# Kernel tuning notes

Hardware: AMD Instinct MI355X
Metric: run time of the kernel (lower is better)

## Reference

```python
import jax, jax.numpy as jnp
import numpy as np

N = 2_000_000
VOXEL_SIZE = (0.1, 0.1, 0.1)
PC_RANGE = (-50.0, -50.0, -5.0, 50.0, 50.0, 3.0)
NUM_BATCHES = 4


def setup_inputs() -> dict:
    key = jax.random.key(0)
    k1, k2 = jax.random.split(key)
    pmin = jnp.array(PC_RANGE[:3], dtype=jnp.float32)
    pmax = jnp.array(PC_RANGE[3:], dtype=jnp.float32)
    # points uniformly distributed over the configured point-cloud range
    points = jax.random.uniform(k1, (N, 3), dtype=jnp.float32, minval=pmin, maxval=pmax)
    batch_indices = jnp.sort(jax.random.randint(k2, (N,), 0, NUM_BATCHES, dtype=jnp.int32))
    return {"points": points, "batch_indices": batch_indices}


def reference(points, batch_indices):
    """Vectorized equivalent of PointVoxelizer.forward.

    Returns fixed-shape (jit-friendly) analogues of the torch outputs:
      voxel_coords   [N, 4] int32  [batch, z, y, x], padded rows = -1
      voxel_features [N, 3] float32 voxel centers, padded rows = 0
      point_to_voxel_map [N] int32, -1 for invalid points
      n_voxels       scalar int32, number of real (non-padding) voxels
    The per-batch torch.unique + offset concatenation is reproduced exactly by
    a single sorted unique over the combined hash batch*GRID + cell_hash,
    since unique sorts and the hash is lexicographic in (batch, x, y, z).
    """
    dtype = points.dtype
    vsize = jnp.array(VOXEL_SIZE, dtype=dtype)
    pmin = jnp.array(PC_RANGE[:3], dtype=dtype)
    pmax = jnp.array(PC_RANGE[3:], dtype=dtype)

    vc = jnp.floor((points - pmin) / vsize).astype(jnp.int32)  # [N,3] (x,y,z)
    grid = jnp.ceil((pmax - pmin) / vsize).astype(jnp.int32)   # [3] = (1000,1000,80)
    valid = jnp.all(vc >= 0, axis=1) & jnp.all(vc < grid, axis=1)  # [N]

    YZ = grid[1] * grid[2]
    GXYZ = grid[0] * YZ  # cells per batch element (8e7 < 2^31/NUM_BATCHES)
    cell_hash = vc[:, 0] * YZ + vc[:, 1] * grid[2] + vc[:, 2]
    SENTINEL = jnp.iinfo(jnp.int32).max
    combined = jnp.where(valid, batch_indices.astype(jnp.int32) * GXYZ + cell_hash, SENTINEL)

    uniq, inv = jnp.unique(combined, return_inverse=True, size=N, fill_value=SENTINEL)
    is_real = uniq != SENTINEL  # padding (and any invalid-point bucket) masked out

    point_to_voxel_map = jnp.where(valid, inv.reshape(-1).astype(jnp.int32), -1)

    b = uniq // GXYZ
    rem = uniq % GXYZ
    x = rem // YZ
    y = (rem % YZ) // grid[2]
    z = rem % grid[2]

    coords_bzyx = jnp.stack([b, z, y, x], axis=1).astype(jnp.int32)  # [N,4]
    voxel_coords = jnp.where(is_real[:, None], coords_bzyx, -1)

    xyz = jnp.stack([x, y, z], axis=1).astype(dtype)
    centers = pmin + (xyz + 0.5) * vsize
    voxel_features = jnp.where(is_real[:, None], centers, jnp.zeros((), dtype))

    n_voxels = is_real.sum().astype(jnp.int32)
    return voxel_coords, voxel_features, point_to_voxel_map, n_voxels
```

## Files before the change

kernel.cpp:

```cpp
#include <hip/hip_runtime.h>


namespace {

constexpr int GX = 1000, GY = 1000, GZ = 80;
constexpr int YZ = GY * GZ;
constexpr int GXYZ = GX * YZ;
constexpr int TOTAL_CELLS = GXYZ * 4;
constexpr int BBITS = 18;
constexpr int BCELLS = 1 << BBITS;
constexpr int NB = (TOTAL_CELLS + BCELLS - 1) >> BBITS;
constexpr int BWORDS = BCELLS / 32;
constexpr int NCHUNK = 1024;
static_assert(NCHUNK % 64 == 0, "k2a wave scan");

constexpr size_t OFF_PK   = 8000000;
constexpr size_t OFF_POS  = 16000000;
constexpr size_t OFF_MVAL = 24000000;
constexpr size_t OFF_HIST = 32000000;
constexpr size_t OFF_TOT  = 38000000;
constexpr size_t OFF_BOFF = 38100000;
constexpr size_t OFF_DCNT = 38200000;

__device__ __forceinline__ int sw(int w) {
  return ((w & 7) << 10) | (w >> 3);
}

__global__ void k1_keys_hist(const float* __restrict__ pts, const int* __restrict__ bi,
                             unsigned* __restrict__ upt, unsigned* __restrict__ hist,
                             int n, int cpb) {
  __shared__ unsigned h[NB];
  const int c = blockIdx.x;
  for (int b = threadIdx.x; b < NB; b += blockDim.x) h[b] = 0;
  __syncthreads();
  const int lo = c * cpb, hi = min(n, lo + cpb);
  for (int i = lo + threadIdx.x; i < hi; i += blockDim.x) {
    float px = pts[3 * i + 0], py = pts[3 * i + 1], pz = pts[3 * i + 2];
    int vx = (int)floorf((px + 50.0f) / 0.1f);
    int vy = (int)floorf((py + 50.0f) / 0.1f);
    int vz = (int)floorf((pz + 5.0f) / 0.1f);
    bool valid = (vx >= 0) & (vy >= 0) & (vz >= 0) & (vx < GX) & (vy < GY) & (vz < GZ);
    unsigned u = 0xFFFFFFFFu;
    if (valid) {
      u = (unsigned)(bi[i] * GXYZ + vx * YZ + vy * GZ + vz);
      atomicAdd(&h[u >> BBITS], 1u);
    }
    upt[i] = u;
  }
  __syncthreads();
  for (int b = threadIdx.x; b < NB; b += blockDim.x)
    hist[(size_t)c * NB + b] = h[b];
}

__global__ void k2a_chunk_pre(unsigned* __restrict__ hist, unsigned* __restrict__ tot) {
  const int wid = (blockIdx.x * blockDim.x + threadIdx.x) >> 6;
  const int lane = threadIdx.x & 63;
  if (wid >= NB) return;
  unsigned run = 0;
  for (int c0 = 0; c0 < NCHUNK; c0 += 64) {
    const size_t idx = (size_t)(c0 + lane) * NB + wid;
    unsigned v = hist[idx];
    unsigned inc = v;
    for (int o = 1; o < 64; o <<= 1) {
      unsigned t = __shfl_up(inc, o);
      if (lane >= o) inc += t;
    }
    hist[idx] = run + inc - v;
    run += __shfl(inc, 63);
  }
  if (lane == 63) tot[wid] = run;
}

__global__ void k2b_scan_tot(const unsigned* __restrict__ tot, unsigned* __restrict__ boff) {
  __shared__ unsigned s[1024];
  const int tid = threadIdx.x;
  unsigned v0 = (2 * tid     < NB) ? tot[2 * tid]     : 0u;
  unsigned v1 = (2 * tid + 1 < NB) ? tot[2 * tid + 1] : 0u;
  unsigned t = v0 + v1;
  s[tid] = t;
  __syncthreads();
  for (int o = 1; o < 1024; o <<= 1) {
    unsigned add = (tid >= o) ? s[tid - o] : 0u;
    __syncthreads();
    s[tid] += add;
    __syncthreads();
  }
  unsigned excl = s[tid] - t;
  if (2 * tid     < NB) boff[2 * tid]     = excl;
  if (2 * tid + 1 < NB) boff[2 * tid + 1] = excl + v0;
  if (tid == 1023) boff[NB] = s[1023];
}

__global__ void k3_scatter(const unsigned* __restrict__ upt, const unsigned* __restrict__ hist,
                           const unsigned* __restrict__ boff, unsigned* __restrict__ pk,
                           unsigned* __restrict__ pos, int n, int cpb) {
  __shared__ unsigned cur[NB];
  const int c = blockIdx.x;
  for (int b = threadIdx.x; b < NB; b += blockDim.x)
    cur[b] = boff[b] + hist[(size_t)c * NB + b];
  __syncthreads();
  const int lo = c * cpb, hi = min(n, lo + cpb);
  for (int i = lo + threadIdx.x; i < hi; i += blockDim.x) {
    unsigned u = upt[i];
    if (u == 0xFFFFFFFFu) continue;
    unsigned p = atomicAdd(&cur[u >> BBITS], 1u);
    pk[p] = u;
    pos[i] = p;
  }
}

__global__ void __launch_bounds__(1024) k4_count(const unsigned* __restrict__ pk,
                                                 const unsigned* __restrict__ boff,
                                                 unsigned* __restrict__ dcnt) {
  __shared__ unsigned bits[BWORDS];
  __shared__ unsigned red[1024];
  const int b = blockIdx.x, tid = threadIdx.x;
  for (int w = tid; w < BWORDS; w += 1024) bits[w] = 0;
  __syncthreads();
  const unsigned lo = boff[b], hi = boff[b + 1];
  const unsigned base = (unsigned)b << BBITS;
  for (unsigned p = lo + tid; p < hi; p += 1024) {
    unsigned local = pk[p] - base;
    atomicOr(&bits[local >> 5], 1u << (local & 31));
  }
  __syncthreads();
  unsigned cnt = 0;
  for (int w = tid; w < BWORDS; w += 1024) cnt += __popc(bits[w]);
  red[tid] = cnt;
  __syncthreads();
  for (int o = 512; o > 0; o >>= 1) {
    if (tid < o) red[tid] += red[tid + o];
    __syncthreads();
  }
  if (tid == 0) dcnt[b] = red[0];
}

__global__ void __launch_bounds__(1024) k6_emit(
    const unsigned* __restrict__ pk, const unsigned* __restrict__ boff,
    const unsigned* __restrict__ dcnt, float* __restrict__ out_coords,
    float* __restrict__ out_feats, float* __restrict__ mapval,
    float* __restrict__ out_nvox, int n) {
  __shared__ unsigned bits[BWORDS];
  __shared__ unsigned wpre[BWORDS];
  __shared__ unsigned s[1024];
  const int tid = threadIdx.x;
  const int bid = blockIdx.x;

  if (bid >= NB) {
    unsigned part = 0;
    for (int k = tid; k < NB; k += 1024) part += dcnt[k];
    s[tid] = part;
    __syncthreads();
    for (int o = 512; o > 0; o >>= 1) {
      if (tid < o) s[tid] += s[tid + o];
      __syncthreads();
    }
    const unsigned nv = s[0];
    if (bid == NB && tid == 0) *out_nvox = (float)nv;
    const int row = (bid - NB) * 1024 + tid;
    if (row < n && (unsigned)row >= nv) {
      float* c = out_coords + (size_t)row * 4;
      c[0] = -1.0f; c[1] = -1.0f; c[2] = -1.0f; c[3] = -1.0f;
      float* f = out_feats + (size_t)row * 3;
      f[0] = 0.0f; f[1] = 0.0f; f[2] = 0.0f;
    }
    return;
  }

  unsigned part = 0;
  for (int k = tid; k < bid; k += 1024) part += dcnt[k];
  s[tid] = part;
  __syncthreads();
  for (int o = 512; o > 0; o >>= 1) {
    if (tid < o) s[tid] += s[tid + o];
    __syncthreads();
  }
  const unsigned drank = s[0];
  __syncthreads();

  for (int w = tid; w < BWORDS; w += 1024) bits[w] = 0;
  __syncthreads();
  const unsigned lo = boff[bid], hi = boff[bid + 1];
  const unsigned base = (unsigned)bid << BBITS;
  for (unsigned p = lo + tid; p < hi; p += 1024) {
    unsigned local = pk[p] - base;
    atomicOr(&bits[sw(local >> 5)], 1u << (local & 31));
  }
  __syncthreads();

  unsigned c8[8];
  unsigned t = 0;
  #pragma unroll
  for (int j = 0; j < 8; j++) {
    unsigned p = __popc(bits[j * 1024 + tid]);
    c8[j] = t;
    t += p;
  }
  s[tid] = t;
  __syncthreads();
  for (int o = 1; o < 1024; o <<= 1) {
    unsigned add = (tid >= o) ? s[tid - o] : 0u;
    __syncthreads();
    s[tid] += add;
    __syncthreads();
  }
  const unsigned excl = s[tid] - t;
  #pragma unroll
  for (int j = 0; j < 8; j++) wpre[j * 1024 + tid] = excl + c8[j];
  __syncthreads();

  #pragma unroll
  for (int j = 0; j < 8; j++) {
    const int slot = j * 1024 + tid;
    unsigned m = bits[slot];
    unsigned r = drank + wpre[slot];
    const unsigned lbase = (unsigned)(tid * 8 + j) << 5;
    while (m) {
      int bit = __ffs(m) - 1;
      m &= m - 1;
      unsigned u = base + lbase + (unsigned)bit;
      int bat = (int)(u / (unsigned)GXYZ);
      int rem = (int)(u % (unsigned)GXYZ);
      int x = rem / YZ, ry = rem % YZ;
      int y = ry / GZ, z = ry % GZ;
      float* cc = out_coords + (size_t)r * 4;
      cc[0] = (float)bat; cc[1] = (float)z; cc[2] = (float)y; cc[3] = (float)x;
      float* ff = out_feats + (size_t)r * 3;
      ff[0] = -50.0f + ((float)x + 0.5f) * 0.1f;
      ff[1] = -50.0f + ((float)y + 0.5f) * 0.1f;
      ff[2] = -5.0f + ((float)z + 0.5f) * 0.1f;
      r++;
    }
  }

  for (unsigned p = lo + tid; p < hi; p += 1024) {
    unsigned local = pk[p] - base;
    int slot = sw((int)(local >> 5));
    unsigned r = drank + wpre[slot] + (unsigned)__popc(bits[slot] & ((1u << (local & 31)) - 1u));
    mapval[p] = (float)r;
  }
}

__global__ void k7_map(const unsigned* __restrict__ upt, const unsigned* __restrict__ pos,
                       const float* __restrict__ mapval, float* __restrict__ out_map, int n) {
  int i = blockIdx.x * blockDim.x + threadIdx.x;
  if (i >= n) return;
  unsigned u = upt[i];
  if (u == 0xFFFFFFFFu) {
    out_map[i] = -1.0f;
    return;
  }
  out_map[i] = mapval[pos[i]];
}

}

extern "C" void kernel_launch(void* const* d_in, const int* in_sizes, int n_in,
                              void* d_out, int out_size, void* d_ws, size_t ws_size,
                              hipStream_t stream) {
  const int N = in_sizes[0] / 3;
  const float* pts = (const float*)d_in[0];
  const int* bi = (const int*)d_in[1];
  float* out = (float*)d_out;

  unsigned* upt = (unsigned*)d_ws;
  unsigned* pk   = (unsigned*)((char*)d_ws + OFF_PK);
  unsigned* pos  = (unsigned*)((char*)d_ws + OFF_POS);
  float*    mval = (float*)((char*)d_ws + OFF_MVAL);
  unsigned* hist = (unsigned*)((char*)d_ws + OFF_HIST);
  unsigned* tot  = (unsigned*)((char*)d_ws + OFF_TOT);
  unsigned* boff = (unsigned*)((char*)d_ws + OFF_BOFF);
  unsigned* dcnt = (unsigned*)((char*)d_ws + OFF_DCNT);

  float* out_coords = out;
  float* out_feats  = out + 4LL * N;
  float* out_map    = out + 7LL * N;
  float* out_nvox   = out + 8LL * N;

  const int cpb = (N + NCHUNK - 1) / NCHUNK;
  const int pad_blocks = (N + 1023) / 1024;

  k1_keys_hist<<<NCHUNK, 256, 0, stream>>>(pts, bi, upt, hist, N, cpb);
  k2a_chunk_pre<<<(NB * 64 + 255) / 256, 256, 0, stream>>>(hist, tot);
  k2b_scan_tot<<<1, 1024, 0, stream>>>(tot, boff);
  k3_scatter<<<NCHUNK, 256, 0, stream>>>(upt, hist, boff, pk, pos, N, cpb);
  k4_count<<<NB, 1024, 0, stream>>>(pk, boff, dcnt);
  k6_emit<<<NB + pad_blocks, 1024, 0, stream>>>(pk, boff, dcnt, out_coords,
                                                out_feats, mval, out_nvox, N);
  k7_map<<<(N + 1023) / 1024, 1024, 0, stream>>>(upt, pos, mval, out_map, N);
}
```

Measured before the change: 197.9 us.

## Merge count and rank passes, compute local ranks, defer global offset to emit

Drops the separate count kernel, which rebuilt each bucket's occupancy bitmap just to count distinct cells. The rank kernel now builds the bitmap once, writes its distinct count plus bucket-local ranks and the sorted distinct keys to workspace. A new lighter emit kernel adds the global prefix and decodes coordinates. The map kernel adds a per-bucket rank from a table. NCHUNK is halved and block sizes shrink to 256. This costs an extra global write and read of the distinct keys and a table lookup per point.

```diff
diff --git a/kernel.cpp b/kernel.cpp
--- a/kernel.cpp
+++ b/kernel.cpp
@@ -11,16 +11,18 @@
 constexpr int BCELLS = 1 << BBITS;
 constexpr int NB = (TOTAL_CELLS + BCELLS - 1) >> BBITS;
 constexpr int BWORDS = BCELLS / 32;
-constexpr int NCHUNK = 1024;
+constexpr int NCHUNK = 512;
 static_assert(NCHUNK % 64 == 0, "k2a wave scan");
 
-constexpr size_t OFF_PK   = 8000000;
-constexpr size_t OFF_POS  = 16000000;
-constexpr size_t OFF_MVAL = 24000000;
-constexpr size_t OFF_HIST = 32000000;
-constexpr size_t OFF_TOT  = 38000000;
-constexpr size_t OFF_BOFF = 38100000;
-constexpr size_t OFF_DCNT = 38200000;
+constexpr size_t OFF_PK    = 8000000;
+constexpr size_t OFF_POS   = 16000000;
+constexpr size_t OFF_MVAL  = 24000000;
+constexpr size_t OFF_DK    = 32000000;
+constexpr size_t OFF_HIST  = 40000000;
+constexpr size_t OFF_TOT   = 43000000;
+constexpr size_t OFF_BOFF  = 43100000;
+constexpr size_t OFF_DCNT  = 43200000;
+constexpr size_t OFF_DRANK = 43300000;
 
 __device__ __forceinline__ int sw(int w) {
   return ((w & 7) << 10) | (w >> 3);
@@ -109,74 +111,15 @@
   }
 }
 
-__global__ void __launch_bounds__(1024) k4_count(const unsigned* __restrict__ pk,
-                                                 const unsigned* __restrict__ boff,
-                                                 unsigned* __restrict__ dcnt) {
-  __shared__ unsigned bits[BWORDS];
-  __shared__ unsigned red[1024];
-  const int b = blockIdx.x, tid = threadIdx.x;
-  for (int w = tid; w < BWORDS; w += 1024) bits[w] = 0;
-  __syncthreads();
-  const unsigned lo = boff[b], hi = boff[b + 1];
-  const unsigned base = (unsigned)b << BBITS;
-  for (unsigned p = lo + tid; p < hi; p += 1024) {
-    unsigned local = pk[p] - base;
-    atomicOr(&bits[local >> 5], 1u << (local & 31));
-  }
-  __syncthreads();
-  unsigned cnt = 0;
-  for (int w = tid; w < BWORDS; w += 1024) cnt += __popc(bits[w]);
-  red[tid] = cnt;
-  __syncthreads();
-  for (int o = 512; o > 0; o >>= 1) {
-    if (tid < o) red[tid] += red[tid + o];
-    __syncthreads();
-  }
-  if (tid == 0) dcnt[b] = red[0];
-}
-
-__global__ void __launch_bounds__(1024) k6_emit(
+__global__ void __launch_bounds__(1024) k4_rank(
     const unsigned* __restrict__ pk, const unsigned* __restrict__ boff,
-    const unsigned* __restrict__ dcnt, float* __restrict__ out_coords,
-    float* __restrict__ out_feats, float* __restrict__ mapval,
-    float* __restrict__ out_nvox, int n) {
+    unsigned* __restrict__ dcnt, unsigned* __restrict__ dk,
+    unsigned* __restrict__ mapval) {
   __shared__ unsigned bits[BWORDS];
   __shared__ unsigned wpre[BWORDS];
   __shared__ unsigned s[1024];
   const int tid = threadIdx.x;
   const int bid = blockIdx.x;
-
-  if (bid >= NB) {
-    unsigned part = 0;
-    for (int k = tid; k < NB; k += 1024) part += dcnt[k];
-    s[tid] = part;
-    __syncthreads();
-    for (int o = 512; o > 0; o >>= 1) {
-      if (tid < o) s[tid] += s[tid + o];
-      __syncthreads();
-    }
-    const unsigned nv = s[0];
-    if (bid == NB && tid == 0) *out_nvox = (float)nv;
-    const int row = (bid - NB) * 1024 + tid;
-    if (row < n && (unsigned)row >= nv) {
-      float* c = out_coords + (size_t)row * 4;
-      c[0] = -1.0f; c[1] = -1.0f; c[2] = -1.0f; c[3] = -1.0f;
-      float* f = out_feats + (size_t)row * 3;
-      f[0] = 0.0f; f[1] = 0.0f; f[2] = 0.0f;
-    }
-    return;
-  }
-
-  unsigned part = 0;
-  for (int k = tid; k < bid; k += 1024) part += dcnt[k];
-  s[tid] = part;
-  __syncthreads();
-  for (int o = 512; o > 0; o >>= 1) {
-    if (tid < o) s[tid] += s[tid + o];
-    __syncthreads();
-  }
-  const unsigned drank = s[0];
-  __syncthreads();
 
   for (int w = tid; w < BWORDS; w += 1024) bits[w] = 0;
   __syncthreads();
@@ -207,28 +150,20 @@
   const unsigned excl = s[tid] - t;
   #pragma unroll
   for (int j = 0; j < 8; j++) wpre[j * 1024 + tid] = excl + c8[j];
-  __syncthreads();
-
+  if (tid == 1023) dcnt[bid] = s[1023];
+  __syncthreads();
+
+  const unsigned dkb = lo;
   #pragma unroll
   for (int j = 0; j < 8; j++) {
     const int slot = j * 1024 + tid;
     unsigned m = bits[slot];
-    unsigned r = drank + wpre[slot];
+    unsigned r = wpre[slot];
     const unsigned lbase = (unsigned)(tid * 8 + j) << 5;
     while (m) {
       int bit = __ffs(m) - 1;
       m &= m - 1;
-      unsigned u = base + lbase + (unsigned)bit;
-      int bat = (int)(u / (unsigned)GXYZ);
-      int rem = (int)(u % (unsigned)GXYZ);
-      int x = rem / YZ, ry = rem % YZ;
-      int y = ry / GZ, z = ry % GZ;
-      float* cc = out_coords + (size_t)r * 4;
-      cc[0] = (float)bat; cc[1] = (float)z; cc[2] = (float)y; cc[3] = (float)x;
-      float* ff = out_feats + (size_t)r * 3;
-      ff[0] = -50.0f + ((float)x + 0.5f) * 0.1f;
-      ff[1] = -50.0f + ((float)y + 0.5f) * 0.1f;
-      ff[2] = -5.0f + ((float)z + 0.5f) * 0.1f;
+      dk[dkb + r] = base + lbase + (unsigned)bit;
       r++;
     }
   }
@@ -236,13 +171,71 @@
   for (unsigned p = lo + tid; p < hi; p += 1024) {
     unsigned local = pk[p] - base;
     int slot = sw((int)(local >> 5));
-    unsigned r = drank + wpre[slot] + (unsigned)__popc(bits[slot] & ((1u << (local & 31)) - 1u));
-    mapval[p] = (float)r;
+    mapval[p] = wpre[slot] + (unsigned)__popc(bits[slot] & ((1u << (local & 31)) - 1u));
+  }
+}
+
+__global__ void k6_emit(const unsigned* __restrict__ dk, const unsigned* __restrict__ boff,
+                        const unsigned* __restrict__ dcnt, unsigned* __restrict__ drank_tbl,
+                        float* __restrict__ out_coords, float* __restrict__ out_feats,
+                        float* __restrict__ out_nvox, int n) {
+  __shared__ unsigned s[256];
+  const int tid = threadIdx.x;
+  const int bid = blockIdx.x;
+
+  if (bid >= NB) {
+    unsigned part = 0;
+    for (int k = tid; k < NB; k += 256) part += dcnt[k];
+    s[tid] = part;
+    __syncthreads();
+    for (int o = 128; o > 0; o >>= 1) {
+      if (tid < o) s[tid] += s[tid + o];
+      __syncthreads();
+    }
+    const unsigned nv = s[0];
+    if (bid == NB && tid == 0) *out_nvox = (float)nv;
+    const int row = (bid - NB) * 256 + tid;
+    if (row < n && (unsigned)row >= nv) {
+      float* c = out_coords + (size_t)row * 4;
+      c[0] = -1.0f; c[1] = -1.0f; c[2] = -1.0f; c[3] = -1.0f;
+      float* f = out_feats + (size_t)row * 3;
+      f[0] = 0.0f; f[1] = 0.0f; f[2] = 0.0f;
+    }
+    return;
+  }
+
+  unsigned part = 0;
+  for (int k = tid; k < bid; k += 256) part += dcnt[k];
+  s[tid] = part;
+  __syncthreads();
+  for (int o = 128; o > 0; o >>= 1) {
+    if (tid < o) s[tid] += s[tid + o];
+    __syncthreads();
+  }
+  const unsigned drank = s[0];
+  if (tid == 0) drank_tbl[bid] = drank;
+
+  const unsigned dc = dcnt[bid];
+  const unsigned dkb = boff[bid];
+  for (unsigned j = tid; j < dc; j += 256) {
+    unsigned u = dk[dkb + j];
+    int bat = (int)(u / (unsigned)GXYZ);
+    int rem = (int)(u % (unsigned)GXYZ);
+    int x = rem / YZ, ry = rem % YZ;
+    int y = ry / GZ, z = ry % GZ;
+    const size_t r = drank + j;
+    float* cc = out_coords + r * 4;
+    cc[0] = (float)bat; cc[1] = (float)z; cc[2] = (float)y; cc[3] = (float)x;
+    float* ff = out_feats + r * 3;
+    ff[0] = -50.0f + ((float)x + 0.5f) * 0.1f;
+    ff[1] = -50.0f + ((float)y + 0.5f) * 0.1f;
+    ff[2] = -5.0f + ((float)z + 0.5f) * 0.1f;
   }
 }
 
 __global__ void k7_map(const unsigned* __restrict__ upt, const unsigned* __restrict__ pos,
-                       const float* __restrict__ mapval, float* __restrict__ out_map, int n) {
+                       const unsigned* __restrict__ mapval, const unsigned* __restrict__ drank_tbl,
+                       float* __restrict__ out_map, int n) {
   int i = blockIdx.x * blockDim.x + threadIdx.x;
   if (i >= n) return;
   unsigned u = upt[i];
@@ -250,7 +243,7 @@
     out_map[i] = -1.0f;
     return;
   }
-  out_map[i] = mapval[pos[i]];
+  out_map[i] = (float)(drank_tbl[u >> BBITS] + mapval[pos[i]]);
 }
 
 }
@@ -263,14 +256,16 @@
   const int* bi = (const int*)d_in[1];
   float* out = (float*)d_out;
 
-  unsigned* upt = (unsigned*)d_ws;
-  unsigned* pk   = (unsigned*)((char*)d_ws + OFF_PK);
-  unsigned* pos  = (unsigned*)((char*)d_ws + OFF_POS);
-  float*    mval = (float*)((char*)d_ws + OFF_MVAL);
-  unsigned* hist = (unsigned*)((char*)d_ws + OFF_HIST);
-  unsigned* tot  = (unsigned*)((char*)d_ws + OFF_TOT);
-  unsigned* boff = (unsigned*)((char*)d_ws + OFF_BOFF);
-  unsigned* dcnt = (unsigned*)((char*)d_ws + OFF_DCNT);
+  unsigned* upt   = (unsigned*)d_ws;
+  unsigned* pk    = (unsigned*)((char*)d_ws + OFF_PK);
+  unsigned* pos   = (unsigned*)((char*)d_ws + OFF_POS);
+  unsigned* mval  = (unsigned*)((char*)d_ws + OFF_MVAL);
+  unsigned* dk    = (unsigned*)((char*)d_ws + OFF_DK);
+  unsigned* hist  = (unsigned*)((char*)d_ws + OFF_HIST);
+  unsigned* tot   = (unsigned*)((char*)d_ws + OFF_TOT);
+  unsigned* boff  = (unsigned*)((char*)d_ws + OFF_BOFF);
+  unsigned* dcnt  = (unsigned*)((char*)d_ws + OFF_DCNT);
+  unsigned* drank = (unsigned*)((char*)d_ws + OFF_DRANK);
 
   float* out_coords = out;
   float* out_feats  = out + 4LL * N;
@@ -278,14 +273,14 @@
   float* out_nvox   = out + 8LL * N;
 
   const int cpb = (N + NCHUNK - 1) / NCHUNK;
-  const int pad_blocks = (N + 1023) / 1024;
+  const int pad_blocks = (N + 255) / 256;
 
   k1_keys_hist<<<NCHUNK, 256, 0, stream>>>(pts, bi, upt, hist, N, cpb);
   k2a_chunk_pre<<<(NB * 64 + 255) / 256, 256, 0, stream>>>(hist, tot);
   k2b_scan_tot<<<1, 1024, 0, stream>>>(tot, boff);
   k3_scatter<<<NCHUNK, 256, 0, stream>>>(upt, hist, boff, pk, pos, N, cpb);
-  k4_count<<<NB, 1024, 0, stream>>>(pk, boff, dcnt);
-  k6_emit<<<NB + pad_blocks, 1024, 0, stream>>>(pk, boff, dcnt, out_coords,
-                                                out_feats, mval, out_nvox, N);
-  k7_map<<<(N + 1023) / 1024, 1024, 0, stream>>>(upt, pos, mval, out_map, N);
-}
+  k4_rank<<<NB, 1024, 0, stream>>>(pk, boff, dcnt, dk, mval);
+  k6_emit<<<NB + pad_blocks, 256, 0, stream>>>(dk, boff, dcnt, drank,
+                                               out_coords, out_feats, out_nvox, N);
+  k7_map<<<(N + 255) / 256, 256, 0, stream>>>(upt, pos, mval, drank, out_map, N);
+}
```

After: 177.6 us. -10.3%, faster.
